# Kernel optimization log

Hardware: AMD Instinct MI355X
Metric: run time of the kernel (lower is better)

The kernel has to match this reference:

```python
import jax, jax.numpy as jnp
import numpy as np

DIM = 1024
HEADS = 16
D_K = DIM // HEADS


def setup_inputs() -> dict:
    key = jax.random.key(0)
    k1, k2, k3, k4 = jax.random.split(key, 4)
    s = 1.0 / np.sqrt(DIM)
    return {
        "x": jax.random.normal(k1, (8, 1024, DIM), dtype=jnp.float32),
        "w_qkv": jax.random.uniform(k2, (DIM, 3 * DIM), dtype=jnp.float32, minval=-s, maxval=s),
        "w_out": jax.random.uniform(k3, (DIM, DIM), dtype=jnp.float32, minval=-s, maxval=s),
        "b_out": jax.random.uniform(k4, (DIM,), dtype=jnp.float32, minval=-s, maxval=s),
    }


def reference(x, w_qkv, w_out, b_out):
    B, N, _ = x.shape
    scale = D_K ** -0.5
    qkv = x @ w_qkv                                   # [B, N, 3*dim]
    q, k, v = jnp.split(qkv, 3, axis=-1)
    # [B, N, dim] -> [B, H, N, d_k]
    def heads(t):
        return t.reshape(B, N, HEADS, D_K).transpose(0, 2, 1, 3)
    q, k, v = heads(q), heads(k), heads(v)
    dots = jnp.einsum("bhnd,bhmd->bhnm", q, k) * scale  # [B, H, N, N]
    attn = jax.nn.softmax(dots, axis=-1)
    out = jnp.einsum("bhnm,bhmd->bhnd", attn, v)        # [B, H, N, d_k]
    out = out.transpose(0, 2, 1, 3).reshape(B, N, HEADS * D_K)
    return out @ w_out + b_out
```

## Files before the change

kernel.cpp:

```cpp
#include <hip/hip_runtime.h>
#include <hip/hip_bf16.h>
#include <math.h>


typedef __attribute__((ext_vector_type(8))) _Float16 f16x8;
typedef __attribute__((ext_vector_type(4))) _Float16 f16x4;
typedef __attribute__((ext_vector_type(4))) float f32x4;
typedef __attribute__((ext_vector_type(16))) float f32x16;
typedef __attribute__((ext_vector_type(4))) unsigned int u32x4;

#define QK_SCALE 0.18033688011112042f

#define GLOBAL_LOAD_LDS16(g, l) \
  __builtin_amdgcn_global_load_lds((const __attribute__((address_space(1))) void*)(g), \
                                   (__attribute__((address_space(3))) void*)(l), 16, 0, 0)

__global__ __launch_bounds__(256) void cast_f16(
    const float* __restrict__ in, _Float16* __restrict__ hi, int n4) {
  int i = blockIdx.x * blockDim.x + threadIdx.x;
  int stride = gridDim.x * blockDim.x;
  for (; i < n4; i += stride) {
    float4 v = ((const float4*)in)[i];
    f16x4 h;
    h[0] = (_Float16)v.x; h[1] = (_Float16)v.y;
    h[2] = (_Float16)v.z; h[3] = (_Float16)v.w;
    ((f16x4*)hi)[i] = h;
  }
}

__global__ __launch_bounds__(256) void cast_t_f16(
    const float* __restrict__ in, int R, int C, _Float16* __restrict__ hi) {
  __shared__ _Float16 hs[64][65];
  const int r0 = blockIdx.y * 64, c0 = blockIdx.x * 64;
  const int t = threadIdx.x;
#pragma unroll
  for (int it = 0; it < 4; ++it) {
    int r = (t >> 4) + it * 16;
    int cc = (t & 15) * 4;
    float4 v = *(const float4*)(in + (size_t)(r0 + r) * C + c0 + cc);
    hs[r][cc + 0] = (_Float16)v.x;
    hs[r][cc + 1] = (_Float16)v.y;
    hs[r][cc + 2] = (_Float16)v.z;
    hs[r][cc + 3] = (_Float16)v.w;
  }
  __syncthreads();
  const int oc = t >> 2;
  const int rr = (t & 3) * 16;
#pragma unroll
  for (int g = 0; g < 2; ++g) {
    f16x8 a;
#pragma unroll
    for (int j = 0; j < 8; ++j) a[j] = hs[rr + g * 8 + j][oc];
    *(f16x8*)(hi + (size_t)(c0 + oc) * R + r0 + rr + g * 8) = a;
  }
}

__global__ __launch_bounds__(256) void gemm1_qkv(
    const _Float16* __restrict__ Ah, const _Float16* __restrict__ Bh,
    _Float16* __restrict__ qkout, _Float16* __restrict__ vTout) {
  __shared__ char lds[34816];
  const int K = 1024;
  const int tid = threadIdx.x;
  const int wave = tid >> 6, lane = tid & 63;
  const int m0 = blockIdx.y * 128, n0 = blockIdx.x * 128;
  const int wr = wave >> 1, wc = wave & 1;

  const int srow = lane >> 2;
  const int sgchunk = (lane & 3) ^ ((srow >> 1) & 3);
  const int lr = lane & 15, kg = lane >> 4;
  const int rdoff = lr * 64 + ((kg ^ ((lr >> 1) & 3)) * 16);

  f32x4 acc[4][4];
#pragma unroll
  for (int m = 0; m < 4; ++m)
#pragma unroll
    for (int n = 0; n < 4; ++n) acc[m][n] = (f32x4){0.f, 0.f, 0.f, 0.f};

  const _Float16* gbase[2];
  gbase[0] = Ah + (size_t)m0 * K;
  gbase[1] = Bh + (size_t)n0 * K;

  for (int k0 = 0; k0 < K; k0 += 32) {
    __syncthreads();
#pragma unroll
    for (int p = 0; p < 2; ++p) {
#pragma unroll
      for (int half = 0; half < 2; ++half) {
        const int r16 = wave * 32 + half * 16;
        const _Float16* g = gbase[p] + (size_t)(r16 + srow) * K + k0 + sgchunk * 8;
        GLOBAL_LOAD_LDS16(g, lds + p * 8192 + r16 * 64);
      }
    }
    __syncthreads();

    f16x8 af[4], bf[4];
#pragma unroll
    for (int m = 0; m < 4; ++m)
      af[m] = *(const f16x8*)(lds + 0 * 8192 + (wr * 64 + m * 16) * 64 + rdoff);
#pragma unroll
    for (int n = 0; n < 4; ++n)
      bf[n] = *(const f16x8*)(lds + 1 * 8192 + (wc * 64 + n * 16) * 64 + rdoff);
#pragma unroll
    for (int m = 0; m < 4; ++m)
#pragma unroll
      for (int n = 0; n < 4; ++n)
        acc[m][n] = __builtin_amdgcn_mfma_f32_16x16x32_f16(af[m], bf[n], acc[m][n], 0, 0, 0);
  }

  const int crow = (lane >> 4) * 4, ccol = lane & 15;
  if (n0 < 2048) {
    const float qsc = (n0 < 1024) ? (float)QK_SCALE : 1.0f;
#pragma unroll
    for (int m = 0; m < 4; ++m) {
#pragma unroll
      for (int n = 0; n < 4; ++n) {
        const int rbase = m0 + wr * 64 + m * 16 + crow;
        const int c = n0 + wc * 64 + n * 16 + ccol;
#pragma unroll
        for (int i = 0; i < 4; ++i)
          qkout[(size_t)(rbase + i) * 2048 + c] = (_Float16)(acc[m][n][i] * qsc);
      }
    }
  } else {
    __syncthreads();
    _Float16* lv = (_Float16*)lds;
#pragma unroll
    for (int m = 0; m < 4; ++m)
#pragma unroll
      for (int n = 0; n < 4; ++n) {
        const int cc = wc * 64 + n * 16 + ccol;
#pragma unroll
        for (int i = 0; i < 4; ++i) {
          const int r = wr * 64 + m * 16 + crow + i;
          lv[cc * 136 + r] = (_Float16)acc[m][n][i];
        }
      }
    __syncthreads();
    const int bb = m0 >> 10, seq0 = m0 & 1023;
    const int hbase = (n0 - 2048) >> 6;
#pragma unroll
    for (int it = 0; it < 8; ++it) {
      const int idx = tid + it * 256;
      const int cc = idx >> 4, ch = idx & 15;
      f16x8 v = *(const f16x8*)(lv + cc * 136 + ch * 8);
      const int hh = hbase + (cc >> 6), d = cc & 63;
      *(f16x8*)(vTout + (((size_t)bb * 16 + hh) * 64 + d) * 1024 + seq0 + ch * 8) = v;
    }
  }
}

__global__ __launch_bounds__(256) void attn_mfma(
    const _Float16* __restrict__ qk,
    const _Float16* __restrict__ vT,
    _Float16* __restrict__ ao) {
  const int hb   = blockIdx.x;
  const int h    = hb >> 3;
  const int b    = hb & 7;
  const int band = blockIdx.y;
  const int tid  = threadIdx.x;
  const int wave = tid >> 6;
  const int lane = tid & 63;
  const int l31  = lane & 31;
  const int hi   = lane >> 5;
  const int kswz = (l31 & 7) << 4;

  __shared__ _Float16 Ks[2][64 * 64];
  __shared__ _Float16 Vt[2][64 * 64];

  const _Float16* vbase = vT + ((size_t)(b * 16 + h) * 64) * 1024;

  const int qrow_g = b * 1024 + band * 128 + wave * 32 + l31;
  f16x8 qf[4];
#pragma unroll
  for (int c = 0; c < 4; ++c)
    qf[c] = *(const f16x8*)(qk + (size_t)qrow_g * 2048 + h * 64 + c * 16 + hi * 8);

  f16x8 vones;
#pragma unroll
  for (int j = 0; j < 8; ++j) vones[j] = (_Float16)1.0f;

  f32x16 accO0 = {0}, accO1 = {0}, accL = {0};

  const int srow8 = (lane >> 3);
  const int slot  = lane & 7;

  auto stage_t = [&](int t, int buf) {
#pragma unroll
    for (int it = 0; it < 2; ++it) {
      const int r  = wave * 8 + srow8 + it * 32;
      const int gc = slot ^ (r & 7);
      const _Float16* gk = qk + (size_t)(b * 1024 + t * 64 + r) * 2048 +
                           1024 + h * 64 + gc * 8;
      const _Float16* gv = vbase + (size_t)r * 1024 + t * 64 + gc * 8;
      char* dk = (char*)&Ks[buf][0] + (wave * 8 + it * 32) * 128;
      char* dv = (char*)&Vt[buf][0] + (wave * 8 + it * 32) * 128;
      GLOBAL_LOAD_LDS16(gk, dk);
      GLOBAL_LOAD_LDS16(gv, dv);
    }
  };

  stage_t(0, 0);

  for (int t = 0; t < 16; ++t) {
    __syncthreads();
    if (t < 15) stage_t(t + 1, (t + 1) & 1);
    const int buf = t & 1;
    const char* ksb = (const char*)&Ks[buf][0];
    const char* vtb = (const char*)&Vt[buf][0];

    f32x16 accS0 = {0}, accS1 = {0};
    __builtin_amdgcn_s_setprio(1);
#pragma unroll
    for (int c = 0; c < 4; ++c) {
      f16x8 ka0 = *(const f16x8*)(ksb + l31 * 128 + ((c * 32 + hi * 16) ^ kswz));
      f16x8 ka1 = *(const f16x8*)(ksb + (l31 + 32) * 128 + ((c * 32 + hi * 16) ^ kswz));
      accS0 = __builtin_amdgcn_mfma_f32_32x32x16_f16(ka0, qf[c], accS0, 0, 0, 0);
      accS1 = __builtin_amdgcn_mfma_f32_32x32x16_f16(ka1, qf[c], accS1, 0, 0, 0);
    }
    __builtin_amdgcn_s_setprio(0);

#pragma unroll
    for (int c = 0; c < 4; ++c) {
      float e[8];
#pragma unroll
      for (int k = 0; k < 8; ++k)
        e[k] = __builtin_exp2f((c < 2) ? accS0[(c & 1) * 8 + k]
                                       : accS1[(c & 1) * 8 + k]);
      unsigned q0a = __builtin_bit_cast(unsigned, __builtin_amdgcn_cvt_pkrtz(e[0], e[1]));
      unsigned q0b = __builtin_bit_cast(unsigned, __builtin_amdgcn_cvt_pkrtz(e[2], e[3]));
      unsigned q1a = __builtin_bit_cast(unsigned, __builtin_amdgcn_cvt_pkrtz(e[4], e[5]));
      unsigned q1b = __builtin_bit_cast(unsigned, __builtin_amdgcn_cvt_pkrtz(e[6], e[7]));
      unsigned send_a = hi ? q0a : q1a;
      unsigned send_b = hi ? q0b : q1b;
      unsigned recv_a = __shfl_xor(send_a, 32);
      unsigned recv_b = __shfl_xor(send_b, 32);
      u32x4 pu;
      pu[0] = hi ? recv_a : q0a;
      pu[1] = hi ? recv_b : q0b;
      pu[2] = hi ? q1a : recv_a;
      pu[3] = hi ? q1b : recv_b;
      f16x8 pa = __builtin_bit_cast(f16x8, pu);

      const int kchunk = ((2 * c + hi) * 16) ^ kswz;
      f16x8 vb0 = *(const f16x8*)(vtb + l31 * 128 + kchunk);
      f16x8 vb1 = *(const f16x8*)(vtb + (l31 + 32) * 128 + kchunk);
      __builtin_amdgcn_s_setprio(1);
      accO0 = __builtin_amdgcn_mfma_f32_32x32x16_f16(pa, vb0, accO0, 0, 0, 0);
      accO1 = __builtin_amdgcn_mfma_f32_32x32x16_f16(pa, vb1, accO1, 0, 0, 0);
      accL  = __builtin_amdgcn_mfma_f32_32x32x16_f16(pa, vones, accL, 0, 0, 0);
      __builtin_amdgcn_s_setprio(0);
    }
  }

#pragma unroll
  for (int reg = 0; reg < 16; ++reg) {
    const int qr = (reg & 3) + 8 * (reg >> 2) + 4 * hi;
    const float il = 1.f / accL[reg];
    const size_t grow = (size_t)(b * 1024 + band * 128 + wave * 32 + qr) * 1024 + h * 64;
    ao[grow + l31]      = (_Float16)(accO0[reg] * il);
    ao[grow + 32 + l31] = (_Float16)(accO1[reg] * il);
  }
}

__global__ __launch_bounds__(256) void gemm2_out(
    const _Float16* __restrict__ A,
    const _Float16* __restrict__ B,
    float* __restrict__ C, const float* __restrict__ bias) {
  __shared__ char lds[2 * 8192];
  const int K = 1024;
  const int tid = threadIdx.x;
  const int wave = tid >> 6, lane = tid & 63;
  const int m0 = blockIdx.y * 128, n0 = blockIdx.x * 128;
  const int wr = wave >> 1, wc = wave & 1;

  const int srow = lane >> 2;
  const int sgchunk = (lane & 3) ^ ((srow >> 1) & 3);
  const int lr = lane & 15, kg = lane >> 4;
  const int rdoff = lr * 64 + ((kg ^ ((lr >> 1) & 3)) * 16);

  f32x4 acc[4][4];
#pragma unroll
  for (int m = 0; m < 4; ++m)
#pragma unroll
    for (int n = 0; n < 4; ++n) acc[m][n] = (f32x4){0.f, 0.f, 0.f, 0.f};

  const _Float16* gbase[2];
  gbase[0] = A + (size_t)m0 * K;
  gbase[1] = B + (size_t)n0 * K;

  for (int k0 = 0; k0 < K; k0 += 32) {
    __syncthreads();
#pragma unroll
    for (int p = 0; p < 2; ++p) {
#pragma unroll
      for (int half = 0; half < 2; ++half) {
        const int r16 = wave * 32 + half * 16;
        const _Float16* g = gbase[p] + (size_t)(r16 + srow) * K + k0 + sgchunk * 8;
        GLOBAL_LOAD_LDS16(g, lds + p * 8192 + r16 * 64);
      }
    }
    __syncthreads();

    f16x8 af[4], bf[4];
#pragma unroll
    for (int m = 0; m < 4; ++m)
      af[m] = *(const f16x8*)(lds + 0 * 8192 + (wr * 64 + m * 16) * 64 + rdoff);
#pragma unroll
    for (int n = 0; n < 4; ++n)
      bf[n] = *(const f16x8*)(lds + 1 * 8192 + (wc * 64 + n * 16) * 64 + rdoff);
#pragma unroll
    for (int m = 0; m < 4; ++m)
#pragma unroll
      for (int n = 0; n < 4; ++n)
        acc[m][n] = __builtin_amdgcn_mfma_f32_16x16x32_f16(af[m], bf[n], acc[m][n], 0, 0, 0);
  }

  const int crow = (lane >> 4) * 4, ccol = lane & 15;
#pragma unroll
  for (int m = 0; m < 4; ++m) {
#pragma unroll
    for (int n = 0; n < 4; ++n) {
      const int rbase = m0 + wr * 64 + m * 16 + crow;
      const int c = n0 + wc * 64 + n * 16 + ccol;
      const float bv = bias[c];
#pragma unroll
      for (int i = 0; i < 4; ++i)
        C[(size_t)(rbase + i) * 1024 + c] = acc[m][n][i] + bv;
    }
  }
}

extern "C" void kernel_launch(void* const* d_in, const int* in_sizes, int n_in,
                              void* d_out, int out_size, void* d_ws, size_t ws_size,
                              hipStream_t stream) {
  const float* x     = (const float*)d_in[0];
  const float* w_qkv = (const float*)d_in[1];
  const float* w_out = (const float*)d_in[2];
  const float* b_out = (const float*)d_in[3];
  float* out = (float*)d_out;

  char* ws = (char*)d_ws;
  _Float16* xh  = (_Float16*)(ws);
  _Float16* ao  = xh;
  _Float16* wqT = (_Float16*)(ws + (32u << 20));
  _Float16* woT = (_Float16*)(ws + (44u << 20));
  _Float16* qkp = (_Float16*)(ws + (48u << 20));
  _Float16* vT  = (_Float16*)(ws + (80u << 20));

  cast_f16<<<2048, 256, 0, stream>>>(x, xh, 8192 * 1024 / 4);
  cast_t_f16<<<dim3(48, 16), 256, 0, stream>>>(w_qkv, 1024, 3072, wqT);
  cast_t_f16<<<dim3(16, 16), 256, 0, stream>>>(w_out, 1024, 1024, woT);

  gemm1_qkv<<<dim3(24, 64), 256, 0, stream>>>(xh, wqT, qkp, vT);

  attn_mfma<<<dim3(128, 8), 256, 0, stream>>>(qkp, vT, ao);

  gemm2_out<<<dim3(8, 64), 256, 0, stream>>>(ao, woT, out, b_out);
}
```

Measured before the change: 180.1 us.

## Load K and V fragments directly from global memory instead of LDS staging

The attention kernel no longer stages K and V^T tiles into double-buffered shared memory with async global-to-LDS loads and block barriers. Each wave now loads its own MFMA operand fragments straight from global memory into registers every iteration. This removes LDS traffic, swizzling and __syncthreads, but the four waves of a block each fetch the same K/V tile, so global/L2 traffic rises by about four times. The loads also lose the prefetch overlap with compute and add register pressure.

```diff
diff --git a/kernel.cpp b/kernel.cpp
--- a/kernel.cpp
+++ b/kernel.cpp
@@ -162,12 +162,6 @@
   const int lane = tid & 63;
   const int l31  = lane & 31;
   const int hi   = lane >> 5;
-  const int kswz = (l31 & 7) << 4;
-
-  __shared__ _Float16 Ks[2][64 * 64];
-  __shared__ _Float16 Vt[2][64 * 64];
-
-  const _Float16* vbase = vT + ((size_t)(b * 16 + h) * 64) * 1024;
 
   const int qrow_g = b * 1024 + band * 128 + wave * 32 + l31;
   f16x8 qf[4];
@@ -175,47 +169,38 @@
   for (int c = 0; c < 4; ++c)
     qf[c] = *(const f16x8*)(qk + (size_t)qrow_g * 2048 + h * 64 + c * 16 + hi * 8);
 
+  const _Float16* kbase0 = qk + (size_t)(b * 1024 + l31) * 2048 + 1024 + h * 64 + hi * 8;
+  const _Float16* kbase1 = kbase0 + (size_t)32 * 2048;
+  const _Float16* vbase0 = vT + ((size_t)(b * 16 + h) * 64 + l31) * 1024 + hi * 8;
+  const _Float16* vbase1 = vbase0 + (size_t)32 * 1024;
+
   f16x8 vones;
 #pragma unroll
   for (int j = 0; j < 8; ++j) vones[j] = (_Float16)1.0f;
 
   f32x16 accO0 = {0}, accO1 = {0}, accL = {0};
 
-  const int srow8 = (lane >> 3);
-  const int slot  = lane & 7;
-
-  auto stage_t = [&](int t, int buf) {
-#pragma unroll
-    for (int it = 0; it < 2; ++it) {
-      const int r  = wave * 8 + srow8 + it * 32;
-      const int gc = slot ^ (r & 7);
-      const _Float16* gk = qk + (size_t)(b * 1024 + t * 64 + r) * 2048 +
-                           1024 + h * 64 + gc * 8;
-      const _Float16* gv = vbase + (size_t)r * 1024 + t * 64 + gc * 8;
-      char* dk = (char*)&Ks[buf][0] + (wave * 8 + it * 32) * 128;
-      char* dv = (char*)&Vt[buf][0] + (wave * 8 + it * 32) * 128;
-      GLOBAL_LOAD_LDS16(gk, dk);
-      GLOBAL_LOAD_LDS16(gv, dv);
-    }
-  };
-
-  stage_t(0, 0);
-
   for (int t = 0; t < 16; ++t) {
-    __syncthreads();
-    if (t < 15) stage_t(t + 1, (t + 1) & 1);
-    const int buf = t & 1;
-    const char* ksb = (const char*)&Ks[buf][0];
-    const char* vtb = (const char*)&Vt[buf][0];
+    const _Float16* kp0 = kbase0 + (size_t)t * (64 * 2048);
+    const _Float16* kp1 = kbase1 + (size_t)t * (64 * 2048);
+    const _Float16* vp0 = vbase0 + t * 64;
+    const _Float16* vp1 = vbase1 + t * 64;
+
+    f16x8 kf0[4], kf1[4], vf0[4], vf1[4];
+#pragma unroll
+    for (int c = 0; c < 4; ++c) {
+      kf0[c] = *(const f16x8*)(kp0 + c * 16);
+      kf1[c] = *(const f16x8*)(kp1 + c * 16);
+      vf0[c] = *(const f16x8*)(vp0 + c * 16);
+      vf1[c] = *(const f16x8*)(vp1 + c * 16);
+    }
 
     f32x16 accS0 = {0}, accS1 = {0};
     __builtin_amdgcn_s_setprio(1);
 #pragma unroll
     for (int c = 0; c < 4; ++c) {
-      f16x8 ka0 = *(const f16x8*)(ksb + l31 * 128 + ((c * 32 + hi * 16) ^ kswz));
-      f16x8 ka1 = *(const f16x8*)(ksb + (l31 + 32) * 128 + ((c * 32 + hi * 16) ^ kswz));
-      accS0 = __builtin_amdgcn_mfma_f32_32x32x16_f16(ka0, qf[c], accS0, 0, 0, 0);
-      accS1 = __builtin_amdgcn_mfma_f32_32x32x16_f16(ka1, qf[c], accS1, 0, 0, 0);
+      accS0 = __builtin_amdgcn_mfma_f32_32x32x16_f16(kf0[c], qf[c], accS0, 0, 0, 0);
+      accS1 = __builtin_amdgcn_mfma_f32_32x32x16_f16(kf1[c], qf[c], accS1, 0, 0, 0);
     }
     __builtin_amdgcn_s_setprio(0);
 
@@ -241,12 +226,9 @@
       pu[3] = hi ? q1b : recv_b;
       f16x8 pa = __builtin_bit_cast(f16x8, pu);
 
-      const int kchunk = ((2 * c + hi) * 16) ^ kswz;
-      f16x8 vb0 = *(const f16x8*)(vtb + l31 * 128 + kchunk);
-      f16x8 vb1 = *(const f16x8*)(vtb + (l31 + 32) * 128 + kchunk);
       __builtin_amdgcn_s_setprio(1);
-      accO0 = __builtin_amdgcn_mfma_f32_32x32x16_f16(pa, vb0, accO0, 0, 0, 0);
-      accO1 = __builtin_amdgcn_mfma_f32_32x32x16_f16(pa, vb1, accO1, 0, 0, 0);
+      accO0 = __builtin_amdgcn_mfma_f32_32x32x16_f16(pa, vf0[c], accO0, 0, 0, 0);
+      accO1 = __builtin_amdgcn_mfma_f32_32x32x16_f16(pa, vf1[c], accO1, 0, 0, 0);
       accL  = __builtin_amdgcn_mfma_f32_32x32x16_f16(pa, vones, accL, 0, 0, 0);
       __builtin_amdgcn_s_setprio(0);
     }
```

Result: slower. 234.7 us (+30.3%).

## Merge cast kernels into one launch and double K-tile depth in QKV GEMM

Applied to the files above, without the earlier changes.

Fuses the three fp32-to-fp16 cast kernels (x cast plus two transposed weight casts) into one kernel that dispatches on block index, which removes two launches. The QKV GEMM now stages a K=64 slice per iteration instead of 32, with a new XOR swizzle over 8 chunks per 128-byte row. This halves the number of barrier pairs and gives two MFMA sub-steps per load. LDS use rises to 32KB for the A/B tiles, which still fits inside the existing 34816-byte buffer.

```diff
diff --git a/kernel.cpp b/kernel.cpp
--- a/kernel.cpp
+++ b/kernel.cpp
@@ -15,24 +15,41 @@
   __builtin_amdgcn_global_load_lds((const __attribute__((address_space(1))) void*)(g), \
                                    (__attribute__((address_space(3))) void*)(l), 16, 0, 0)
 
-__global__ __launch_bounds__(256) void cast_f16(
-    const float* __restrict__ in, _Float16* __restrict__ hi, int n4) {
-  int i = blockIdx.x * blockDim.x + threadIdx.x;
-  int stride = gridDim.x * blockDim.x;
-  for (; i < n4; i += stride) {
-    float4 v = ((const float4*)in)[i];
-    f16x4 h;
-    h[0] = (_Float16)v.x; h[1] = (_Float16)v.y;
-    h[2] = (_Float16)v.z; h[3] = (_Float16)v.w;
-    ((f16x4*)hi)[i] = h;
-  }
-}
-
-__global__ __launch_bounds__(256) void cast_t_f16(
-    const float* __restrict__ in, int R, int C, _Float16* __restrict__ hi) {
+__global__ __launch_bounds__(256) void cast_all(
+    const float* __restrict__ x, _Float16* __restrict__ xh,
+    const float* __restrict__ w_qkv, _Float16* __restrict__ wqT,
+    const float* __restrict__ w_out, _Float16* __restrict__ woT) {
   __shared__ _Float16 hs[64][65];
-  const int r0 = blockIdx.y * 64, c0 = blockIdx.x * 64;
+  const int blk = blockIdx.x;
   const int t = threadIdx.x;
+
+  if (blk < 2048) {
+    const int n4 = 8192 * 1024 / 4;
+    int i = blk * 256 + t;
+    const int stride = 2048 * 256;
+    for (; i < n4; i += stride) {
+      float4 v = ((const float4*)x)[i];
+      f16x4 h;
+      h[0] = (_Float16)v.x; h[1] = (_Float16)v.y;
+      h[2] = (_Float16)v.z; h[3] = (_Float16)v.w;
+      ((f16x4*)xh)[i] = h;
+    }
+    return;
+  }
+
+  const float* in;
+  _Float16* hi;
+  int R, C, bx, by;
+  if (blk < 2048 + 768) {
+    const int id = blk - 2048;
+    in = w_qkv; hi = wqT; R = 1024; C = 3072;
+    bx = id % 48; by = id / 48;
+  } else {
+    const int id = blk - 2816;
+    in = w_out; hi = woT; R = 1024; C = 1024;
+    bx = id % 16; by = id / 16;
+  }
+  const int r0 = by * 64, c0 = bx * 64;
 #pragma unroll
   for (int it = 0; it < 4; ++it) {
     int r = (t >> 4) + it * 16;
@@ -65,10 +82,10 @@
   const int m0 = blockIdx.y * 128, n0 = blockIdx.x * 128;
   const int wr = wave >> 1, wc = wave & 1;
 
-  const int srow = lane >> 2;
-  const int sgchunk = (lane & 3) ^ ((srow >> 1) & 3);
+  const int srow_off = lane >> 3;
+  const int slot     = lane & 7;
+
   const int lr = lane & 15, kg = lane >> 4;
-  const int rdoff = lr * 64 + ((kg ^ ((lr >> 1) & 3)) * 16);
 
   f32x4 acc[4][4];
 #pragma unroll
@@ -80,31 +97,41 @@
   gbase[0] = Ah + (size_t)m0 * K;
   gbase[1] = Bh + (size_t)n0 * K;
 
-  for (int k0 = 0; k0 < K; k0 += 32) {
+  for (int k0 = 0; k0 < K; k0 += 64) {
     __syncthreads();
 #pragma unroll
     for (int p = 0; p < 2; ++p) {
 #pragma unroll
-      for (int half = 0; half < 2; ++half) {
-        const int r16 = wave * 32 + half * 16;
-        const _Float16* g = gbase[p] + (size_t)(r16 + srow) * K + k0 + sgchunk * 8;
-        GLOBAL_LOAD_LDS16(g, lds + p * 8192 + r16 * 64);
-      }
-    }
-    __syncthreads();
-
-    f16x8 af[4], bf[4];
-#pragma unroll
-    for (int m = 0; m < 4; ++m)
-      af[m] = *(const f16x8*)(lds + 0 * 8192 + (wr * 64 + m * 16) * 64 + rdoff);
-#pragma unroll
-    for (int n = 0; n < 4; ++n)
-      bf[n] = *(const f16x8*)(lds + 1 * 8192 + (wc * 64 + n * 16) * 64 + rdoff);
-#pragma unroll
-    for (int m = 0; m < 4; ++m)
-#pragma unroll
-      for (int n = 0; n < 4; ++n)
-        acc[m][n] = __builtin_amdgcn_mfma_f32_16x16x32_f16(af[m], bf[n], acc[m][n], 0, 0, 0);
+      for (int it = 0; it < 4; ++it) {
+        const int rbase = wave * 32 + it * 8;
+        const int r  = rbase + srow_off;
+        const int gc = slot ^ (r & 7);
+        const _Float16* g = gbase[p] + (size_t)r * K + k0 + gc * 8;
+        GLOBAL_LOAD_LDS16(g, lds + p * 16384 + rbase * 128);
+      }
+    }
+    __syncthreads();
+
+#pragma unroll
+    for (int s2 = 0; s2 < 2; ++s2) {
+      f16x8 af[4], bf[4];
+      const int c = s2 * 4 + kg;
+#pragma unroll
+      for (int m = 0; m < 4; ++m) {
+        const int e = wr * 64 + m * 16 + lr;
+        af[m] = *(const f16x8*)(lds + 0 * 16384 + e * 128 + ((c ^ (e & 7)) * 16));
+      }
+#pragma unroll
+      for (int n = 0; n < 4; ++n) {
+        const int e = wc * 64 + n * 16 + lr;
+        bf[n] = *(const f16x8*)(lds + 1 * 16384 + e * 128 + ((c ^ (e & 7)) * 16));
+      }
+#pragma unroll
+      for (int m = 0; m < 4; ++m)
+#pragma unroll
+        for (int n = 0; n < 4; ++n)
+          acc[m][n] = __builtin_amdgcn_mfma_f32_16x16x32_f16(af[m], bf[n], acc[m][n], 0, 0, 0);
+    }
   }
 
   const int crow = (lane >> 4) * 4, ccol = lane & 15;
@@ -115,10 +142,10 @@
 #pragma unroll
       for (int n = 0; n < 4; ++n) {
         const int rbase = m0 + wr * 64 + m * 16 + crow;
-        const int c = n0 + wc * 64 + n * 16 + ccol;
+        const int cc = n0 + wc * 64 + n * 16 + ccol;
 #pragma unroll
         for (int i = 0; i < 4; ++i)
-          qkout[(size_t)(rbase + i) * 2048 + c] = (_Float16)(acc[m][n][i] * qsc);
+          qkout[(size_t)(rbase + i) * 2048 + cc] = (_Float16)(acc[m][n][i] * qsc);
       }
     }
   } else {
@@ -347,9 +374,7 @@
   _Float16* qkp = (_Float16*)(ws + (48u << 20));
   _Float16* vT  = (_Float16*)(ws + (80u << 20));
 
-  cast_f16<<<2048, 256, 0, stream>>>(x, xh, 8192 * 1024 / 4);
-  cast_t_f16<<<dim3(48, 16), 256, 0, stream>>>(w_qkv, 1024, 3072, wqT);
-  cast_t_f16<<<dim3(16, 16), 256, 0, stream>>>(w_out, 1024, 1024, woT);
+  cast_all<<<3072, 256, 0, stream>>>(x, xh, w_qkv, wqT, w_out, woT);
 
   gemm1_qkv<<<dim3(24, 64), 256, 0, stream>>>(xh, wqT, qkp, vT);
 
```

New measurement: 176.5 us. 2.0% less time.
